# Kernel tuning notes

Hardware: AMD Instinct MI355X
Metric: run time of the kernel (lower is better)

Reference implementation:

```python
import jax, jax.numpy as jnp
import numpy as np

N_ELEMENTS = 64  # StructureElementLayer(n_elements=64)


def setup_inputs() -> dict:
    key = jax.random.key(0)
    k1, k2 = jax.random.split(key)
    # x: [N, C, T, V] skeleton sequence (batch, coord channels, time, joints)
    x = jax.random.normal(k1, (256, 3, 256, 25), dtype=jnp.float32)
    # StructureElementLayer parameters (torch.rand init / ones*3 init)
    centres = jax.random.uniform(k2, (N_ELEMENTS, 2), dtype=jnp.float32)
    sharpness = jnp.ones((N_ELEMENTS, 2), dtype=jnp.float32) * 3.0
    return {"x": x, "centres": centres, "sharpness": sharpness}


def _mst_deaths(D):
    """Dim-0 Vietoris-Rips persistence deaths == MST edge weights (Prim's algorithm).

    D: [n, n] symmetric distance matrix. Returns [n-1] finite death values
    (births are all 0; the single essential (0, inf) pair contributes
    exp(-inf)=0 to the structure-element layer and is dropped).
    """
    n = D.shape[0]
    in_tree = jnp.zeros((n,), dtype=bool).at[0].set(True)
    dist = D[0]  # min distance from each node to the current tree

    def step(carry, _):
        in_tree, dist = carry
        d = jnp.where(in_tree, jnp.inf, dist)
        j = jnp.argmin(d)
        w = d[j]
        in_tree = in_tree.at[j].set(True)
        dist = jnp.minimum(dist, D[j])
        return (in_tree, dist), w

    (_, _), deaths = jax.lax.scan(step, (in_tree, dist), None, length=n - 1)
    return deaths


def _forward(x, centres, sharpness):
    xm = x.mean(1)                                  # [N, T, V]
    diff = xm[..., :, None] - xm[..., None, :]      # [N, T, V, V] pairwise joint diffs
    diff = diff.mean(-3)                            # [N, V, V]
    feat = jnp.linalg.norm(diff, axis=1)            # [N, V]  (torch.norm(., 2, dim=1))
    feat = (feat - feat.min()) / (feat.max() - feat.min())
    # Euclidean distance matrix of the N points in V-dim space (grad-safe sqrt)
    sq = jnp.sum(feat * feat, axis=1)
    D2 = sq[:, None] + sq[None, :] - 2.0 * (feat @ feat.T)
    D2 = jnp.maximum(D2, 0.0)
    D = jnp.where(D2 > 0.0, jnp.sqrt(jnp.where(D2 > 0.0, D2, 1.0)), 0.0)
    deaths = _mst_deaths(D)                         # [N-1]
    diag = jnp.stack([jnp.zeros_like(deaths), deaths], axis=-1)  # [N-1, 2] (birth, death)
    # StructureElementLayer: sum_i exp(-sum_d (p_id - c_kd)^2 * s_kd^2)
    d2 = (diag[:, None, :] - centres[None, :, :]) ** 2            # [N-1, K, 2]
    out = jnp.exp(-(d2 * (sharpness ** 2)).sum(-1)).sum(0)        # [K]
    return out


def reference(x, centres, sharpness):
    return _forward(x, centres, sharpness)
```

## Files before the change

kernel.cpp:

```cpp
#include <hip/hip_runtime.h>
#include <hip/hip_fp16.h>


#define WS_M    0
#define WS_MM   25600
#define WS_RK   28672
#define WS_DTH  29696
#define WS_NCDC 30720
#define WS_D16  65536
#define WS_MP   196608

#define INF32 0xFFFFFFFFu
#define MPSTR 132

__global__ void k_mean(const float* __restrict__ x, float* __restrict__ m,
                       unsigned int* __restrict__ Mp) {
    const int n = blockIdx.x;
    const int tid = threadIdx.x;
    if (tid < 66) Mp[n * 66 + tid] = INF32;
    __shared__ float sums[25];
    if (tid < 25) sums[tid] = 0.0f;
    __syncthreads();
    if (tid < 200) {
        const float* base = x + (long)n * 19200 + 4 * tid;
        float a0 = 0.f, a1 = 0.f, a2 = 0.f, a3 = 0.f;
        #pragma unroll
        for (int i = 0; i < 24; ++i) {
            float4 v = *reinterpret_cast<const float4*>(base + 800 * i);
            a0 += v.x; a1 += v.y; a2 += v.z; a3 += v.w;
        }
        const int v0 = (4 * tid) % 25;
        atomicAdd(&sums[v0], a0);
        atomicAdd(&sums[(v0 + 1) % 25], a1);
        atomicAdd(&sums[(v0 + 2) % 25], a2);
        atomicAdd(&sums[(v0 + 3) % 25], a3);
    }
    __syncthreads();
    if (tid < 25) m[n * 25 + tid] = sums[tid] * (1.0f / 768.0f);
}

template <int CTRL>
__device__ __forceinline__ unsigned int dpp_min_step(unsigned int v) {
    unsigned int t = (unsigned int)__builtin_amdgcn_update_dpp(
        (int)0xFFFFFFFF, (int)v, CTRL, 0xF, 0xF, false);
    return (t < v) ? t : v;
}

__global__ void __launch_bounds__(256) k_dist(const float* __restrict__ m,
                                              unsigned short* __restrict__ D16,
                                              unsigned int* __restrict__ rowKeyG,
                                              unsigned int* __restrict__ mm) {
    __shared__ float mS[6400];
    __shared__ float featS[6400];
    __shared__ unsigned int bmin, bmax;
    __shared__ unsigned int wred[4];
    const int i = blockIdx.x;
    const int t = threadIdx.x;
    if (t == 0) { bmin = 0x7F800000u; bmax = 0u; }
    #pragma unroll
    for (int it = 0; it < 7; ++it) {
        int o = it * 256 + t;
        if (o < 1600) reinterpret_cast<float4*>(mS)[o] =
            reinterpret_cast<const float4*>(m)[o];
    }
    __syncthreads();
    float r[25];
    #pragma unroll
    for (int v = 0; v < 25; ++v) r[v] = mS[t * 25 + v];
    float S1 = 0.f, S2 = 0.f;
    #pragma unroll
    for (int v = 0; v < 25; ++v) { S1 += r[v]; S2 += r[v] * r[v]; }
    float fmn = 1e30f, fmx = -1e30f;
    #pragma unroll
    for (int w = 0; w < 25; ++w) {
        float q = S2 - 2.f * r[w] * S1 + 25.f * r[w] * r[w];
        q = fmaxf(q, 0.f);
        float f = sqrtf(q);
        featS[t * 25 + w] = f;
        fmn = fminf(fmn, f); fmx = fmaxf(fmx, f);
    }
    if (i == 0) {
        atomicMin(&bmin, __float_as_uint(fmn));
        atomicMax(&bmax, __float_as_uint(fmx));
    }
    __syncthreads();
    if (i == 0 && t == 0) { mm[0] = bmin; mm[1] = bmax; }
    float fi[25];
    #pragma unroll
    for (int v = 0; v < 25; ++v) fi[v] = featS[i * 25 + v];
    float s = 0.f;
    #pragma unroll
    for (int v = 0; v < 25; ++v) { float d = fi[v] - featS[t * 25 + v]; s += d * d; }
    const unsigned int w16 = (unsigned int)__half_as_ushort(__float2half(s));
    D16[i * 256 + t] = (unsigned short)w16;
    const unsigned int lo = (i < t) ? i : t, hi = (i < t) ? t : i;
    unsigned int key = (t == i) ? INF32 : ((w16 << 16) | (lo << 8) | hi);
    key = dpp_min_step<0x111>(key);
    key = dpp_min_step<0x112>(key);
    key = dpp_min_step<0x114>(key);
    key = dpp_min_step<0x118>(key);
    key = dpp_min_step<0x142>(key);
    key = dpp_min_step<0x143>(key);
    if ((t & 63) == 63) wred[t >> 6] = key;
    __syncthreads();
    if (t == 0) {
        unsigned int b0 = wred[0] < wred[1] ? wred[0] : wred[1];
        unsigned int b1 = wred[2] < wred[3] ? wred[2] : wred[3];
        rowKeyG[i] = b0 < b1 ? b0 : b1;
    }
}

template <bool RECORD>
__device__ __forceinline__ void wave0_phase(int n, int lane,
        unsigned int* rowKeyS, unsigned char* parentS, unsigned char* newidS,
        unsigned char* cmapS, float* deaths, unsigned int* ncS, unsigned int* dcS) {
    unsigned int par[4];
    #pragma unroll
    for (int s = 0; s < 4; ++s) {
        const int i = lane + 64 * s;
        if (i < n) {
            const unsigned int rk = rowKeyS[i];
            const unsigned int u = (rk >> 8) & 0xFFu, v = rk & 0xFFu;
            unsigned int p = (u == (unsigned int)i) ? v : u;
            if (rk == INF32) p = (unsigned int)i;
            par[s] = p;
            parentS[i] = (unsigned char)p;
        }
    }
    #pragma unroll
    for (int s = 0; s < 4; ++s) {
        const int i = lane + 64 * s;
        if (i < n) {
            const unsigned int p = par[s];
            if (p != (unsigned int)i) {
                if (parentS[p] == (unsigned char)i && (unsigned int)i < p) {
                    parentS[i] = (unsigned char)i;
                } else if (RECORD) {
                    const unsigned int d = atomicAdd(dcS, 1u);
                    const unsigned int rk = rowKeyS[i];
                    deaths[d] = sqrtf(__half2float(__ushort_as_half(
                        (unsigned short)(rk >> 16))));
                }
            }
        }
    }
    for (;;) {
        bool ch = false;
        #pragma unroll
        for (int s = 0; s < 4; ++s) {
            const int i = lane + 64 * s;
            if (i < n) {
                const unsigned char p0 = parentS[i];
                const unsigned char np = parentS[p0];
                if (np != p0) { ch = true; parentS[i] = np; }
            }
        }
        if (__ballot(ch) == 0ull) break;
    }
    bool isr[4];
    #pragma unroll
    for (int s = 0; s < 4; ++s) {
        const int i = lane + 64 * s;
        isr[s] = (i < n) && (parentS[i] == (unsigned char)i);
    }
    unsigned int base = 0;
    const unsigned long long below = (1ull << lane) - 1ull;
    #pragma unroll
    for (int s = 0; s < 4; ++s) {
        const unsigned long long mask = __ballot(isr[s]);
        if (isr[s]) {
            const int i = lane + 64 * s;
            newidS[i] = (unsigned char)(base + __popcll(mask & below));
        }
        base += (unsigned int)__popcll(mask);
    }
    if (lane == 0) *ncS = base;
    #pragma unroll
    for (int s = 0; s < 4; ++s) {
        const int i = lane + 64 * s;
        if (i < n) cmapS[i] = newidS[parentS[i]];
    }
}

__global__ void __launch_bounds__(256) k_contract(const unsigned short* __restrict__ D16g,
                                                  const unsigned int* __restrict__ rowKeyG,
                                                  unsigned int* __restrict__ Mp,
                                                  float* __restrict__ deathsG,
                                                  unsigned int* __restrict__ ncdcG) {
    __shared__ unsigned int rowKeyS[256];
    __shared__ unsigned char parentS[256], newidS[256], cmapS[256];
    __shared__ unsigned int ncS, dcS;
    __shared__ float deathsS[256];
    const int tid = threadIdx.x;
    const int b = blockIdx.x;
    rowKeyS[tid] = rowKeyG[tid];
    if (tid == 0) dcS = 0;
    __syncthreads();
    if (tid < 64) {
        if (b == 0)
            wave0_phase<true>(256, tid, rowKeyS, parentS, newidS, cmapS,
                              deathsS, &ncS, &dcS);
        else
            wave0_phase<false>(256, tid, rowKeyS, parentS, newidS, cmapS,
                               nullptr, &ncS, nullptr);
    }
    __syncthreads();
    if (b == 0) {
        if (tid < dcS) deathsG[tid] = deathsS[tid];
        if (tid == 0) { ncdcG[0] = ncS; ncdcG[1] = dcS; }
    }
    const unsigned int ca = cmapS[b];
    const unsigned int cb = cmapS[tid];
    if (ca != cb) {
        const unsigned int w16 = (unsigned int)D16g[b * 256 + tid];
        const unsigned int lo = ca < cb ? ca : cb;
        const unsigned int hi = ca < cb ? cb : ca;
        atomicMin(&Mp[ca * MPSTR + cb], (w16 << 16) | (lo << 8) | hi);
    }
}

#define SA 132
#define SB 68
#define OFF_B (128 * SA)

__global__ void __launch_bounds__(1024) k_mst(const unsigned int* __restrict__ Mp,
                                              const float* __restrict__ deathsG,
                                              const unsigned int* __restrict__ ncdcG,
                                              const unsigned int* __restrict__ mm,
                                              const float* __restrict__ centres,
                                              const float* __restrict__ sharp,
                                              float* __restrict__ out) {
    __shared__ unsigned int Mb[128 * SA + 64 * SB];
    __shared__ unsigned int rowKeyS[256];
    __shared__ unsigned char parentS[256], newidS[256], cmapS[256];
    __shared__ unsigned int ncS, dcS;
    __shared__ float deaths[256];
    __shared__ float outpart[1024];
    const int tid = threadIdx.x;

    if (tid == 0) { ncS = ncdcG[0]; dcS = ncdcG[1]; }
    if (tid < 256) deaths[tid] = deathsG[tid];
    __syncthreads();
    int n = (int)ncS;

    for (int idx = tid; idx < n * SA; idx += 1024) Mb[idx] = Mp[idx];
    __syncthreads();

    int srcOff = 0, srcStr = SA, dstOff = OFF_B, dstStr = SB;
    for (int round = 0; round < 12 && n > 1; ++round) {
        if (tid < n) rowKeyS[tid] = INF32;
        __syncthreads();
        if (tid < 8 * n) {
            const int a = tid >> 3, sub = tid & 7;
            const unsigned int* row = &Mb[srcOff + a * srcStr];
            unsigned int best = INF32;
            for (int b2 = sub; b2 < n; b2 += 8) {
                const unsigned int v = row[b2];
                best = v < best ? v : best;
            }
            if (best != INF32) atomicMin(&rowKeyS[a], best);
        }
        __syncthreads();
        if (tid < 64)
            wave0_phase<true>(n, tid, rowKeyS, parentS, newidS, cmapS,
                              deaths, &ncS, &dcS);
        __syncthreads();
        const int nc = (int)ncS;
        if (nc > 1) {
            for (int w = tid; w < nc * dstStr; w += 1024) Mb[dstOff + w] = INF32;
            __syncthreads();
            if (tid < 8 * n) {
                const int a = tid >> 3, sub = tid & 7;
                const unsigned int ca = cmapS[a];
                const unsigned int* row = &Mb[srcOff + a * srcStr];
                for (int b2 = sub; b2 < n; b2 += 8) {
                    const unsigned int cb = cmapS[b2];
                    const unsigned int v = row[b2];
                    if (ca != cb && v != INF32) {
                        const unsigned int lo = ca < cb ? ca : cb;
                        const unsigned int hi = ca < cb ? cb : ca;
                        atomicMin(&Mb[dstOff + ca * dstStr + cb],
                                  (v & 0xFFFF0000u) | (lo << 8) | hi);
                    }
                }
            }
            __syncthreads();
        }
        const int t1 = srcOff; srcOff = dstOff; dstOff = t1;
        const int t2 = srcStr; srcStr = dstStr; dstStr = t2;
        n = nc;
    }

    const float mn = __uint_as_float(mm[0]);
    const float mx = __uint_as_float(mm[1]);
    const float inv = 1.0f / (mx - mn);
    const int k = tid & 63;
    const int part = tid >> 6;
    const float c0 = centres[2 * k], c1 = centres[2 * k + 1];
    const float s0 = sharp[2 * k],   s1 = sharp[2 * k + 1];
    const float t0 = c0 * c0 * s0 * s0;
    const float s1sq = s1 * s1;
    float acc = 0.f;
    for (int idx = part; idx < 255; idx += 16) {
        const float d = deaths[idx] * inv - c1;
        acc += __expf(-(t0 + d * d * s1sq));
    }
    outpart[tid] = acc;
    __syncthreads();
    if (tid < 64) {
        float s = 0.f;
        #pragma unroll
        for (int pp = 0; pp < 16; ++pp) s += outpart[tid + 64 * pp];
        out[tid] = s;
    }
}

extern "C" void kernel_launch(void* const* d_in, const int* in_sizes, int n_in,
                              void* d_out, int out_size, void* d_ws, size_t ws_size,
                              hipStream_t stream) {
    const float* x       = (const float*)d_in[0];
    const float* centres = (const float*)d_in[1];
    const float* sharp   = (const float*)d_in[2];
    float* out = (float*)d_out;
    char* ws = (char*)d_ws;
    float*          m    = (float*)(ws + WS_M);
    unsigned int*   mm   = (unsigned int*)(ws + WS_MM);
    unsigned int*   rk   = (unsigned int*)(ws + WS_RK);
    float*          dth  = (float*)(ws + WS_DTH);
    unsigned int*   ncdc = (unsigned int*)(ws + WS_NCDC);
    unsigned short* D16  = (unsigned short*)(ws + WS_D16);
    unsigned int*   Mp   = (unsigned int*)(ws + WS_MP);

    k_mean<<<256, 256, 0, stream>>>(x, m, Mp);
    k_dist<<<256, 256, 0, stream>>>(m, D16, rk, mm);
    k_contract<<<256, 256, 0, stream>>>(D16, rk, Mp, dth, ncdc);
    k_mst<<<1, 1024, 0, stream>>>(Mp, dth, ncdc, mm, centres, sharp, out);
}
```

Measured before the change: 93.14 us.

## Replace Boruvka contraction with single-block Prim MST overlapping distance production

Fuses the feature normalisation into the mean kernel, then runs one 1024-thread block that computes the pairwise distance matrix into LDS with 15 producer waves while wave 0 runs Prim's algorithm, spinning on per-row ready flags. This removes two kernel launches, the global distance and contraction buffers, and the multi-round Boruvka contraction. In exchange, the MST becomes 255 serial wave-level argmin steps, and the kernel depends on a large LDS allocation and intra-block spin-waiting.

```diff
diff --git a/kernel.cpp b/kernel.cpp
--- a/kernel.cpp
+++ b/kernel.cpp
@@ -2,24 +2,24 @@
 #include <hip/hip_fp16.h>
 
 
-#define WS_M    0
-#define WS_MM   25600
-#define WS_RK   28672
-#define WS_DTH  29696
-#define WS_NCDC 30720
-#define WS_D16  65536
-#define WS_MP   196608
+#define WS_FEAT 0
+#define WS_FMN  26624
+#define WS_FMX  27648
 
 #define INF32 0xFFFFFFFFu
-#define MPSTR 132
-
-__global__ void k_mean(const float* __restrict__ x, float* __restrict__ m,
-                       unsigned int* __restrict__ Mp) {
+
+__global__ void __launch_bounds__(256) k_feat(const float* __restrict__ x,
+                                              float* __restrict__ featG,
+                                              float* __restrict__ fmnG,
+                                              float* __restrict__ fmxG) {
+    __shared__ float sums[25];
+    __shared__ float mrow[25];
+    __shared__ float S12[2];
+    __shared__ unsigned int bmn, bmx;
     const int n = blockIdx.x;
     const int tid = threadIdx.x;
-    if (tid < 66) Mp[n * 66 + tid] = INF32;
-    __shared__ float sums[25];
     if (tid < 25) sums[tid] = 0.0f;
+    if (tid == 0) { bmn = 0x7F800000u; bmx = 0u; }
     __syncthreads();
     if (tid < 200) {
         const float* base = x + (long)n * 19200 + 4 * tid;
@@ -36,7 +36,26 @@
         atomicAdd(&sums[(v0 + 3) % 25], a3);
     }
     __syncthreads();
-    if (tid < 25) m[n * 25 + tid] = sums[tid] * (1.0f / 768.0f);
+    if (tid < 25) mrow[tid] = sums[tid] * (1.0f / 768.0f);
+    __syncthreads();
+    if (tid == 0) {
+        float S1 = 0.f, S2 = 0.f;
+        #pragma unroll
+        for (int v = 0; v < 25; ++v) { S1 += mrow[v]; S2 += mrow[v] * mrow[v]; }
+        S12[0] = S1; S12[1] = S2;
+    }
+    __syncthreads();
+    if (tid < 25) {
+        const float r = mrow[tid];
+        float q = S12[1] - 2.f * r * S12[0] + 25.f * r * r;
+        q = fmaxf(q, 0.f);
+        const float f = sqrtf(q);
+        featG[n * 26 + tid] = f;
+        atomicMin(&bmn, __float_as_uint(f));
+        atomicMax(&bmx, __float_as_uint(f));
+    }
+    __syncthreads();
+    if (tid == 0) { fmnG[n] = __uint_as_float(bmn); fmxG[n] = __uint_as_float(bmx); }
 }
 
 template <int CTRL>
@@ -46,271 +65,138 @@
     return (t < v) ? t : v;
 }
 
-__global__ void __launch_bounds__(256) k_dist(const float* __restrict__ m,
-                                              unsigned short* __restrict__ D16,
-                                              unsigned int* __restrict__ rowKeyG,
-                                              unsigned int* __restrict__ mm) {
-    __shared__ float mS[6400];
-    __shared__ float featS[6400];
-    __shared__ unsigned int bmin, bmax;
-    __shared__ unsigned int wred[4];
-    const int i = blockIdx.x;
-    const int t = threadIdx.x;
-    if (t == 0) { bmin = 0x7F800000u; bmax = 0u; }
-    #pragma unroll
-    for (int it = 0; it < 7; ++it) {
-        int o = it * 256 + t;
-        if (o < 1600) reinterpret_cast<float4*>(mS)[o] =
-            reinterpret_cast<const float4*>(m)[o];
-    }
-    __syncthreads();
-    float r[25];
-    #pragma unroll
-    for (int v = 0; v < 25; ++v) r[v] = mS[t * 25 + v];
-    float S1 = 0.f, S2 = 0.f;
-    #pragma unroll
-    for (int v = 0; v < 25; ++v) { S1 += r[v]; S2 += r[v] * r[v]; }
-    float fmn = 1e30f, fmx = -1e30f;
-    #pragma unroll
-    for (int w = 0; w < 25; ++w) {
-        float q = S2 - 2.f * r[w] * S1 + 25.f * r[w] * r[w];
-        q = fmaxf(q, 0.f);
-        float f = sqrtf(q);
-        featS[t * 25 + w] = f;
-        fmn = fminf(fmn, f); fmx = fmaxf(fmx, f);
-    }
-    if (i == 0) {
-        atomicMin(&bmin, __float_as_uint(fmn));
-        atomicMax(&bmax, __float_as_uint(fmx));
-    }
-    __syncthreads();
-    if (i == 0 && t == 0) { mm[0] = bmin; mm[1] = bmax; }
-    float fi[25];
-    #pragma unroll
-    for (int v = 0; v < 25; ++v) fi[v] = featS[i * 25 + v];
-    float s = 0.f;
-    #pragma unroll
-    for (int v = 0; v < 25; ++v) { float d = fi[v] - featS[t * 25 + v]; s += d * d; }
-    const unsigned int w16 = (unsigned int)__half_as_ushort(__float2half(s));
-    D16[i * 256 + t] = (unsigned short)w16;
-    const unsigned int lo = (i < t) ? i : t, hi = (i < t) ? t : i;
-    unsigned int key = (t == i) ? INF32 : ((w16 << 16) | (lo << 8) | hi);
-    key = dpp_min_step<0x111>(key);
-    key = dpp_min_step<0x112>(key);
-    key = dpp_min_step<0x114>(key);
-    key = dpp_min_step<0x118>(key);
-    key = dpp_min_step<0x142>(key);
-    key = dpp_min_step<0x143>(key);
-    if ((t & 63) == 63) wred[t >> 6] = key;
-    __syncthreads();
-    if (t == 0) {
-        unsigned int b0 = wred[0] < wred[1] ? wred[0] : wred[1];
-        unsigned int b1 = wred[2] < wred[3] ? wred[2] : wred[3];
-        rowKeyG[i] = b0 < b1 ? b0 : b1;
-    }
-}
-
-template <bool RECORD>
-__device__ __forceinline__ void wave0_phase(int n, int lane,
-        unsigned int* rowKeyS, unsigned char* parentS, unsigned char* newidS,
-        unsigned char* cmapS, float* deaths, unsigned int* ncS, unsigned int* dcS) {
-    unsigned int par[4];
-    #pragma unroll
-    for (int s = 0; s < 4; ++s) {
-        const int i = lane + 64 * s;
-        if (i < n) {
-            const unsigned int rk = rowKeyS[i];
-            const unsigned int u = (rk >> 8) & 0xFFu, v = rk & 0xFFu;
-            unsigned int p = (u == (unsigned int)i) ? v : u;
-            if (rk == INF32) p = (unsigned int)i;
-            par[s] = p;
-            parentS[i] = (unsigned char)p;
-        }
-    }
-    #pragma unroll
-    for (int s = 0; s < 4; ++s) {
-        const int i = lane + 64 * s;
-        if (i < n) {
-            const unsigned int p = par[s];
-            if (p != (unsigned int)i) {
-                if (parentS[p] == (unsigned char)i && (unsigned int)i < p) {
-                    parentS[i] = (unsigned char)i;
-                } else if (RECORD) {
-                    const unsigned int d = atomicAdd(dcS, 1u);
-                    const unsigned int rk = rowKeyS[i];
-                    deaths[d] = sqrtf(__half2float(__ushort_as_half(
-                        (unsigned short)(rk >> 16))));
-                }
+__global__ void __launch_bounds__(1024) k_topo(const float* __restrict__ featG,
+                                               const float* __restrict__ fmnG,
+                                               const float* __restrict__ fmxG,
+                                               const float* __restrict__ centres,
+                                               const float* __restrict__ sharp,
+                                               float* __restrict__ out) {
+    __shared__ __align__(16) union { float featS[6656]; float outpart[1024]; } FS;
+    __shared__ unsigned short D16h[65536];
+    __shared__ unsigned int rowReady[256];
+    __shared__ float deathsS[256];
+    __shared__ unsigned int mmS[2];
+    const int tid = threadIdx.x;
+
+    if (tid == 0) { mmS[0] = 0x7F800000u; mmS[1] = 0u; }
+    if (tid < 256) rowReady[tid] = 0u;
+    __syncthreads();
+    for (int o = tid; o < 1664; o += 1024)
+        reinterpret_cast<float4*>(FS.featS)[o] =
+            reinterpret_cast<const float4*>(featG)[o];
+    if (tid < 256) {
+        atomicMin(&mmS[0], __float_as_uint(fmnG[tid]));
+        atomicMax(&mmS[1], __float_as_uint(fmxG[tid]));
+    }
+    __syncthreads();
+
+    const int wv = tid >> 6, lane = tid & 63;
+    volatile unsigned int* rr = rowReady;
+
+    if (wv == 0) {
+        { unsigned g = 0;
+          while (rr[0] == 0u) { __builtin_amdgcn_s_sleep(2); if (++g > (1u<<20)) break; } }
+        __threadfence_block();
+        unsigned int d0, d1, d2_, d3;
+        {
+            const unsigned int h0 = D16h[lane];
+            const unsigned int h1 = D16h[64 + lane];
+            const unsigned int h2 = D16h[128 + lane];
+            const unsigned int h3 = D16h[192 + lane];
+            d0 = (h0 << 16) | (unsigned)lane;
+            d1 = (h1 << 16) | (unsigned)(64 + lane);
+            d2_ = (h2 << 16) | (unsigned)(128 + lane);
+            d3 = (h3 << 16) | (unsigned)(192 + lane);
+        }
+        unsigned int tb = 0;
+        if (lane == 0) { tb = 1u; d0 = INF32; }
+        for (int it = 0; it < 255; ++it) {
+            unsigned int a = d0 < d1 ? d0 : d1;
+            unsigned int b = d2_ < d3 ? d2_ : d3;
+            unsigned int key = a < b ? a : b;
+            key = dpp_min_step<0x111>(key);
+            key = dpp_min_step<0x112>(key);
+            key = dpp_min_step<0x114>(key);
+            key = dpp_min_step<0x118>(key);
+            key = dpp_min_step<0x142>(key);
+            key = dpp_min_step<0x143>(key);
+            const unsigned int best = (unsigned int)__builtin_amdgcn_readlane((int)key, 63);
+            const unsigned int j = best & 0xFFu;
+            if (lane == 0)
+                deathsS[it] = sqrtf(__half2float(__ushort_as_half(
+                    (unsigned short)(best >> 16))));
+            const unsigned int lj = j & 63u;
+            const unsigned int slot = j >> 6;
+            if ((unsigned)lane == lj) {
+                tb |= (1u << slot);
+                if (slot == 0u) d0 = INF32;
+                else if (slot == 1u) d1 = INF32;
+                else if (slot == 2u) d2_ = INF32;
+                else d3 = INF32;
             }
-        }
-    }
-    for (;;) {
-        bool ch = false;
-        #pragma unroll
-        for (int s = 0; s < 4; ++s) {
-            const int i = lane + 64 * s;
-            if (i < n) {
-                const unsigned char p0 = parentS[i];
-                const unsigned char np = parentS[p0];
-                if (np != p0) { ch = true; parentS[i] = np; }
+            { unsigned g = 0;
+              while (rr[j] == 0u) { __builtin_amdgcn_s_sleep(2); if (++g > (1u<<20)) break; } }
+            __threadfence_block();
+            const unsigned int rb = j << 8;
+            const unsigned int h0 = D16h[rb + lane];
+            const unsigned int h1 = D16h[rb + 64 + lane];
+            const unsigned int h2 = D16h[rb + 128 + lane];
+            const unsigned int h3 = D16h[rb + 192 + lane];
+            const unsigned int n0 = (h0 << 16) | (unsigned)lane;
+            const unsigned int n1 = (h1 << 16) | (unsigned)(64 + lane);
+            const unsigned int n2 = (h2 << 16) | (unsigned)(128 + lane);
+            const unsigned int n3 = (h3 << 16) | (unsigned)(192 + lane);
+            d0 = (tb & 1u) ? INF32 : (n0 < d0 ? n0 : d0);
+            d1 = (tb & 2u) ? INF32 : (n1 < d1 ? n1 : d1);
+            d2_ = (tb & 4u) ? INF32 : (n2 < d2_ ? n2 : d2_);
+            d3 = (tb & 8u) ? INF32 : (n3 < d3 ? n3 : d3);
+        }
+    } else {
+        for (int r = wv - 1; r < 256; r += 15) {
+            float fi[25];
+            #pragma unroll
+            for (int v = 0; v < 25; ++v) fi[v] = FS.featS[r * 26 + v];
+            float s0 = 0.f, s1 = 0.f, s2 = 0.f, s3 = 0.f;
+            const int j0 = lane, j1 = 64 + lane, j2 = 128 + lane, j3 = 192 + lane;
+            #pragma unroll
+            for (int v = 0; v < 25; ++v) {
+                const float fv = fi[v];
+                const float e0 = fv - FS.featS[j0 * 26 + v]; s0 += e0 * e0;
+                const float e1 = fv - FS.featS[j1 * 26 + v]; s1 += e1 * e1;
+                const float e2 = fv - FS.featS[j2 * 26 + v]; s2 += e2 * e2;
+                const float e3 = fv - FS.featS[j3 * 26 + v]; s3 += e3 * e3;
             }
-        }
-        if (__ballot(ch) == 0ull) break;
-    }
-    bool isr[4];
-    #pragma unroll
-    for (int s = 0; s < 4; ++s) {
-        const int i = lane + 64 * s;
-        isr[s] = (i < n) && (parentS[i] == (unsigned char)i);
-    }
-    unsigned int base = 0;
-    const unsigned long long below = (1ull << lane) - 1ull;
-    #pragma unroll
-    for (int s = 0; s < 4; ++s) {
-        const unsigned long long mask = __ballot(isr[s]);
-        if (isr[s]) {
-            const int i = lane + 64 * s;
-            newidS[i] = (unsigned char)(base + __popcll(mask & below));
-        }
-        base += (unsigned int)__popcll(mask);
-    }
-    if (lane == 0) *ncS = base;
-    #pragma unroll
-    for (int s = 0; s < 4; ++s) {
-        const int i = lane + 64 * s;
-        if (i < n) cmapS[i] = newidS[parentS[i]];
-    }
-}
-
-__global__ void __launch_bounds__(256) k_contract(const unsigned short* __restrict__ D16g,
-                                                  const unsigned int* __restrict__ rowKeyG,
-                                                  unsigned int* __restrict__ Mp,
-                                                  float* __restrict__ deathsG,
-                                                  unsigned int* __restrict__ ncdcG) {
-    __shared__ unsigned int rowKeyS[256];
-    __shared__ unsigned char parentS[256], newidS[256], cmapS[256];
-    __shared__ unsigned int ncS, dcS;
-    __shared__ float deathsS[256];
-    const int tid = threadIdx.x;
-    const int b = blockIdx.x;
-    rowKeyS[tid] = rowKeyG[tid];
-    if (tid == 0) dcS = 0;
-    __syncthreads();
-    if (tid < 64) {
-        if (b == 0)
-            wave0_phase<true>(256, tid, rowKeyS, parentS, newidS, cmapS,
-                              deathsS, &ncS, &dcS);
-        else
-            wave0_phase<false>(256, tid, rowKeyS, parentS, newidS, cmapS,
-                               nullptr, &ncS, nullptr);
-    }
-    __syncthreads();
-    if (b == 0) {
-        if (tid < dcS) deathsG[tid] = deathsS[tid];
-        if (tid == 0) { ncdcG[0] = ncS; ncdcG[1] = dcS; }
-    }
-    const unsigned int ca = cmapS[b];
-    const unsigned int cb = cmapS[tid];
-    if (ca != cb) {
-        const unsigned int w16 = (unsigned int)D16g[b * 256 + tid];
-        const unsigned int lo = ca < cb ? ca : cb;
-        const unsigned int hi = ca < cb ? cb : ca;
-        atomicMin(&Mp[ca * MPSTR + cb], (w16 << 16) | (lo << 8) | hi);
-    }
-}
-
-#define SA 132
-#define SB 68
-#define OFF_B (128 * SA)
-
-__global__ void __launch_bounds__(1024) k_mst(const unsigned int* __restrict__ Mp,
-                                              const float* __restrict__ deathsG,
-                                              const unsigned int* __restrict__ ncdcG,
-                                              const unsigned int* __restrict__ mm,
-                                              const float* __restrict__ centres,
-                                              const float* __restrict__ sharp,
-                                              float* __restrict__ out) {
-    __shared__ unsigned int Mb[128 * SA + 64 * SB];
-    __shared__ unsigned int rowKeyS[256];
-    __shared__ unsigned char parentS[256], newidS[256], cmapS[256];
-    __shared__ unsigned int ncS, dcS;
-    __shared__ float deaths[256];
-    __shared__ float outpart[1024];
-    const int tid = threadIdx.x;
-
-    if (tid == 0) { ncS = ncdcG[0]; dcS = ncdcG[1]; }
-    if (tid < 256) deaths[tid] = deathsG[tid];
-    __syncthreads();
-    int n = (int)ncS;
-
-    for (int idx = tid; idx < n * SA; idx += 1024) Mb[idx] = Mp[idx];
-    __syncthreads();
-
-    int srcOff = 0, srcStr = SA, dstOff = OFF_B, dstStr = SB;
-    for (int round = 0; round < 12 && n > 1; ++round) {
-        if (tid < n) rowKeyS[tid] = INF32;
-        __syncthreads();
-        if (tid < 8 * n) {
-            const int a = tid >> 3, sub = tid & 7;
-            const unsigned int* row = &Mb[srcOff + a * srcStr];
-            unsigned int best = INF32;
-            for (int b2 = sub; b2 < n; b2 += 8) {
-                const unsigned int v = row[b2];
-                best = v < best ? v : best;
-            }
-            if (best != INF32) atomicMin(&rowKeyS[a], best);
-        }
-        __syncthreads();
-        if (tid < 64)
-            wave0_phase<true>(n, tid, rowKeyS, parentS, newidS, cmapS,
-                              deaths, &ncS, &dcS);
-        __syncthreads();
-        const int nc = (int)ncS;
-        if (nc > 1) {
-            for (int w = tid; w < nc * dstStr; w += 1024) Mb[dstOff + w] = INF32;
-            __syncthreads();
-            if (tid < 8 * n) {
-                const int a = tid >> 3, sub = tid & 7;
-                const unsigned int ca = cmapS[a];
-                const unsigned int* row = &Mb[srcOff + a * srcStr];
-                for (int b2 = sub; b2 < n; b2 += 8) {
-                    const unsigned int cb = cmapS[b2];
-                    const unsigned int v = row[b2];
-                    if (ca != cb && v != INF32) {
-                        const unsigned int lo = ca < cb ? ca : cb;
-                        const unsigned int hi = ca < cb ? cb : ca;
-                        atomicMin(&Mb[dstOff + ca * dstStr + cb],
-                                  (v & 0xFFFF0000u) | (lo << 8) | hi);
-                    }
-                }
-            }
-            __syncthreads();
-        }
-        const int t1 = srcOff; srcOff = dstOff; dstOff = t1;
-        const int t2 = srcStr; srcStr = dstStr; dstStr = t2;
-        n = nc;
-    }
-
-    const float mn = __uint_as_float(mm[0]);
-    const float mx = __uint_as_float(mm[1]);
+            const unsigned int rb = (unsigned)r << 8;
+            D16h[rb + j0] = __half_as_ushort(__float2half(s0));
+            D16h[rb + j1] = __half_as_ushort(__float2half(s1));
+            D16h[rb + j2] = __half_as_ushort(__float2half(s2));
+            D16h[rb + j3] = __half_as_ushort(__float2half(s3));
+            __threadfence_block();
+            if (lane == 0) rr[r] = 1u;
+        }
+    }
+    __syncthreads();
+
+    const float mn = __uint_as_float(mmS[0]);
+    const float mx = __uint_as_float(mmS[1]);
     const float inv = 1.0f / (mx - mn);
     const int k = tid & 63;
     const int part = tid >> 6;
     const float c0 = centres[2 * k], c1 = centres[2 * k + 1];
-    const float s0 = sharp[2 * k],   s1 = sharp[2 * k + 1];
-    const float t0 = c0 * c0 * s0 * s0;
-    const float s1sq = s1 * s1;
+    const float sh0 = sharp[2 * k],  sh1 = sharp[2 * k + 1];
+    const float t0 = c0 * c0 * sh0 * sh0;
+    const float s1sq = sh1 * sh1;
     float acc = 0.f;
     for (int idx = part; idx < 255; idx += 16) {
-        const float d = deaths[idx] * inv - c1;
+        const float d = deathsS[idx] * inv - c1;
         acc += __expf(-(t0 + d * d * s1sq));
     }
-    outpart[tid] = acc;
+    FS.outpart[tid] = acc;
     __syncthreads();
     if (tid < 64) {
         float s = 0.f;
         #pragma unroll
-        for (int pp = 0; pp < 16; ++pp) s += outpart[tid + 64 * pp];
+        for (int pp = 0; pp < 16; ++pp) s += FS.outpart[tid + 64 * pp];
         out[tid] = s;
     }
 }
@@ -323,16 +209,10 @@
     const float* sharp   = (const float*)d_in[2];
     float* out = (float*)d_out;
     char* ws = (char*)d_ws;
-    float*          m    = (float*)(ws + WS_M);
-    unsigned int*   mm   = (unsigned int*)(ws + WS_MM);
-    unsigned int*   rk   = (unsigned int*)(ws + WS_RK);
-    float*          dth  = (float*)(ws + WS_DTH);
-    unsigned int*   ncdc = (unsigned int*)(ws + WS_NCDC);
-    unsigned short* D16  = (unsigned short*)(ws + WS_D16);
-    unsigned int*   Mp   = (unsigned int*)(ws + WS_MP);
-
-    k_mean<<<256, 256, 0, stream>>>(x, m, Mp);
-    k_dist<<<256, 256, 0, stream>>>(m, D16, rk, mm);
-    k_contract<<<256, 256, 0, stream>>>(D16, rk, Mp, dth, ncdc);
-    k_mst<<<1, 1024, 0, stream>>>(Mp, dth, ncdc, mm, centres, sharp, out);
-}
+    float* featG = (float*)(ws + WS_FEAT);
+    float* fmnG  = (float*)(ws + WS_FMN);
+    float* fmxG  = (float*)(ws + WS_FMX);
+
+    k_feat<<<256, 256, 0, stream>>>(x, featG, fmnG, fmxG);
+    k_topo<<<1, 1024, 0, stream>>>(featG, fmnG, fmxG, centres, sharp, out);
+}
```

Measured after the change: 197.9 us. +112.5%, slower.
